# Kernel optimization log

Measured on AMD Instinct MI355X. Metric: run time of the kernel, lower is better.

Reference implementation:

```python
import jax, jax.numpy as jnp
import numpy as np

B, S, D = 16, 2048, 512
SEQ_START = 4
MAX_LEN = 1007
NUM_SEQ = MAX_LEN - SEQ_START  # 1003 rows in sequence_embeddings
VOCAB = 100


def setup_inputs() -> dict:
    key = jax.random.key(0)
    k_x, k_ids, k_pos, k_c, k_s = jax.random.split(key, 5)
    x = jax.random.normal(k_x, (B, S, D), dtype=jnp.float32)
    input_ids = jax.random.randint(k_ids, (B, S), 0, VOCAB, dtype=jnp.int64)
    start_token_id = 5
    # plant exactly one guaranteed start token per row at pos >= SEQ_START
    start_pos = jax.random.randint(k_pos, (B,), SEQ_START, S // 2, dtype=jnp.int64)
    input_ids = input_ids.at[jnp.arange(B), start_pos].set(start_token_id)
    control_emb = jax.random.normal(k_c, (SEQ_START, D), dtype=jnp.float32) * 0.02
    sequence_emb = jax.random.normal(k_s, (NUM_SEQ, D), dtype=jnp.float32) * 0.02
    return {"x": x, "input_ids": input_ids, "start_token_id": start_token_id,
            "control_emb": control_emb, "sequence_emb": sequence_emb}


def reference(x, input_ids, start_token_id, control_emb, sequence_emb):
    Bx, Sx, Dx = x.shape
    pos = jnp.arange(Sx)
    # control embeddings fill positions [0, SEQ_START)
    n_ctrl = control_emb.shape[0]
    ctrl_mask = pos < n_ctrl                                 # [S]
    ctrl_part = control_emb[jnp.clip(pos, 0, n_ctrl - 1)]    # [S, D]
    ctrl_part = jnp.where(ctrl_mask[:, None], ctrl_part, 0.0)
    # sequence embeddings: for each position i, rel = i - (last start pos <= i
    # with start pos >= SEQ_START); later starts overwrite earlier ones,
    # matching the torch loop's overwrite semantics.
    is_start = (input_ids == start_token_id) & (pos[None, :] >= SEQ_START)  # [B, S]
    marker = jnp.where(is_start, pos[None, :], -1)
    last_start = jax.lax.cummax(marker, axis=1)              # [B, S]
    rel = pos[None, :] - last_start                          # [B, S]
    n_seq = sequence_emb.shape[0]
    valid = (last_start >= 0) & (rel < n_seq)                # [B, S]
    seq_part = sequence_emb[jnp.clip(rel, 0, n_seq - 1)]     # [B, S, D]
    pos_emb = jnp.where(valid[:, :, None], seq_part, ctrl_part[None, :, :])
    return x + pos_emb
```

## Files before the change

### kernel.cpp

```cpp
#include <hip/hip_runtime.h>
#include <hip/hip_bf16.h>


#define S_LEN 2048
#define D_DIM 512
#define D4 (D_DIM / 4)
#define SEQ_START 4
#define NUM_SEQ 1003
#define CS 64
#define NCHUNK (S_LEN / CS)
#define THREADS 512
#define NWAVE (THREADS / 64)
#define PER (S_LEN / THREADS)

typedef float f4 __attribute__((ext_vector_type(4)));

__global__ void __launch_bounds__(THREADS)
alpe_fused_kernel(const f4* __restrict__ x,
                  const f4* __restrict__ ctrl,
                  const f4* __restrict__ seq,
                  const int* __restrict__ ids,
                  const int* __restrict__ start_tok,
                  f4* __restrict__ out) {
    const int b   = blockIdx.x / NCHUNK;
    const int cid = blockIdx.x % NCHUNK;
    const int chunk_start = cid * CS;
    const int t = threadIdx.x;
    const int st = *start_tok;

    __shared__ int wmax[NWAVE];
    __shared__ int codes_s[CS];

    int m = -1;
    #pragma unroll
    for (int k = 0; k < PER; ++k) {
        const int j = t * PER + k;
        if (j < chunk_start) {
            const int id = ids[b * S_LEN + j];
            if (id == st && j >= SEQ_START) m = max(m, j);
        }
    }
    #pragma unroll
    for (int off = 32; off >= 1; off >>= 1)
        m = max(m, __shfl_xor(m, off));
    if ((t & 63) == 0) wmax[t >> 6] = m;
    __syncthreads();

    if (t < 64) {
        const int p = chunk_start + t;
        const int id = ids[b * S_LEN + p];
        int mk = (id == st && p >= SEQ_START) ? p : -1;
        #pragma unroll
        for (int off = 1; off < 64; off <<= 1) {
            const int o = __shfl_up(mk, off);
            if (t >= off) mk = max(mk, o);
        }
        int carry = -1;
        #pragma unroll
        for (int w = 0; w < NWAVE; ++w) carry = max(carry, wmax[w]);
        const int last = max(mk, carry);
        int code;
        if (last >= 0) {
            const int rel = p - last;
            code = (rel < NUM_SEQ) ? rel : -1;
        } else {
            code = (p < SEQ_START) ? (-2 - p) : -1;
        }
        codes_s[t] = code;
    }
    __syncthreads();

    const size_t base4 = ((size_t)(b * S_LEN + chunk_start)) * D4;
    #pragma unroll
    for (int it = 0; it < (CS * D4) / THREADS; ++it) {
        const int j  = it * THREADS + t;
        const int sl = j >> 7;
        const int d4 = j & (D4 - 1);
        const int code = codes_s[sl];
        const f4 xv = x[base4 + j];
        f4 e = (f4){0.f, 0.f, 0.f, 0.f};
        if (code >= 0) {
            e = seq[code * D4 + d4];
        } else if (code <= -2) {
            e = ctrl[(-2 - code) * D4 + d4];
        }
        out[base4 + j] = xv + e;
    }
}

extern "C" void kernel_launch(void* const* d_in, const int* in_sizes, int n_in,
                              void* d_out, int out_size, void* d_ws, size_t ws_size,
                              hipStream_t stream) {
    const float* x         = (const float*)d_in[0];
    const int*   input_ids = (const int*)d_in[1];
    const int*   start_tok = (const int*)d_in[2];
    const float* ctrl      = (const float*)d_in[3];
    const float* seq       = (const float*)d_in[4];
    float*       out       = (float*)d_out;

    const int B = in_sizes[1] / S_LEN;
    const int grid = B * NCHUNK;

    alpe_fused_kernel<<<grid, THREADS, 0, stream>>>(
        (const f4*)x, (const f4*)ctrl, (const f4*)seq,
        input_ids, start_tok, (f4*)out);
}
```

Measured before the change: 27.15 us.

## Remove shared-memory syncs, compute codes per wave, and prefetch x rows early

```diff
diff --git a/kernel.cpp b/kernel.cpp
--- a/kernel.cpp
+++ b/kernel.cpp
@@ -3,88 +3,92 @@
 
 
 #define S_LEN 2048
-#define D_DIM 512
-#define D4 (D_DIM / 4)
+#define D4 128
 #define SEQ_START 4
 #define NUM_SEQ 1003
 #define CS 64
 #define NCHUNK (S_LEN / CS)
 #define THREADS 512
-#define NWAVE (THREADS / 64)
-#define PER (S_LEN / THREADS)
+#define ITERS ((CS * D4) / THREADS)
+#define PF 8
+#define IDR 8
 
 typedef float f4 __attribute__((ext_vector_type(4)));
+typedef int   i4 __attribute__((ext_vector_type(4)));
 
-__global__ void __launch_bounds__(THREADS)
-alpe_fused_kernel(const f4* __restrict__ x,
-                  const f4* __restrict__ ctrl,
-                  const f4* __restrict__ seq,
-                  const int* __restrict__ ids,
-                  const int* __restrict__ start_tok,
-                  f4* __restrict__ out) {
+__global__ void __launch_bounds__(THREADS, 4)
+alpe_kernel(const f4* __restrict__ x,
+            const f4* __restrict__ ctrl,
+            const f4* __restrict__ seq,
+            const int* __restrict__ ids,
+            const int* __restrict__ start_tok,
+            f4* __restrict__ out) {
     const int b   = blockIdx.x / NCHUNK;
     const int cid = blockIdx.x % NCHUNK;
     const int chunk_start = cid * CS;
     const int t = threadIdx.x;
+    const int w = t >> 6;
+    const int l = t & 63;
     const int st = *start_tok;
+    const int* __restrict__ idrow = ids + b * S_LEN;
 
-    __shared__ int wmax[NWAVE];
-    __shared__ int codes_s[CS];
+    const int myid = idrow[chunk_start + l];
+    i4 idv[IDR];
+    #pragma unroll
+    for (int r = 0; r < IDR; ++r)
+        idv[r] = *(const i4*)&idrow[r * 256 + l * 4];
 
-    int m = -1;
+    const size_t base4 = (size_t)(b * S_LEN + chunk_start) * D4;
+    f4 xp[PF];
     #pragma unroll
-    for (int k = 0; k < PER; ++k) {
-        const int j = t * PER + k;
-        if (j < chunk_start) {
-            const int id = ids[b * S_LEN + j];
-            if (id == st && j >= SEQ_START) m = max(m, j);
+    for (int i = 0; i < PF; ++i)
+        xp[i] = x[base4 + i * THREADS + t];
+
+    int pm = -1;
+    #pragma unroll
+    for (int r = 0; r < IDR; ++r) {
+        #pragma unroll
+        for (int k = 0; k < 4; ++k) {
+            const int j = r * 256 + l * 4 + k;
+            const int id = idv[r][k];
+            if (id == st && j >= SEQ_START && j < chunk_start) pm = max(pm, j);
         }
     }
     #pragma unroll
     for (int off = 32; off >= 1; off >>= 1)
-        m = max(m, __shfl_xor(m, off));
-    if ((t & 63) == 0) wmax[t >> 6] = m;
-    __syncthreads();
+        pm = max(pm, __shfl_xor(pm, off));
 
-    if (t < 64) {
-        const int p = chunk_start + t;
-        const int id = ids[b * S_LEN + p];
-        int mk = (id == st && p >= SEQ_START) ? p : -1;
-        #pragma unroll
-        for (int off = 1; off < 64; off <<= 1) {
-            const int o = __shfl_up(mk, off);
-            if (t >= off) mk = max(mk, o);
-        }
-        int carry = -1;
-        #pragma unroll
-        for (int w = 0; w < NWAVE; ++w) carry = max(carry, wmax[w]);
-        const int last = max(mk, carry);
-        int code;
-        if (last >= 0) {
-            const int rel = p - last;
-            code = (rel < NUM_SEQ) ? rel : -1;
-        } else {
-            code = (p < SEQ_START) ? (-2 - p) : -1;
-        }
-        codes_s[t] = code;
+    const int p = chunk_start + l;
+    int mk = (myid == st && p >= SEQ_START) ? p : -1;
+    #pragma unroll
+    for (int off = 1; off < 64; off <<= 1) {
+        const int o = __shfl_up(mk, off);
+        if (l >= off) mk = max(mk, o);
     }
-    __syncthreads();
+    const int last = max(mk, pm);
+    int mycode;
+    if (last >= 0) {
+        const int rel = p - last;
+        mycode = (rel < NUM_SEQ) ? rel : -1;
+    } else {
+        mycode = (p < SEQ_START) ? (-2 - p) : -1;
+    }
 
-    const size_t base4 = ((size_t)(b * S_LEN + chunk_start)) * D4;
+    const int d4w = ((w & 1) << 6) | l;
+    const int rsel = w >> 1;
     #pragma unroll
-    for (int it = 0; it < (CS * D4) / THREADS; ++it) {
-        const int j  = it * THREADS + t;
-        const int sl = j >> 7;
-        const int d4 = j & (D4 - 1);
-        const int code = codes_s[sl];
-        const f4 xv = x[base4 + j];
+    for (int it = 0; it < ITERS; ++it) {
+        const f4 xv = xp[it & (PF - 1)];
+        if (it + PF < ITERS)
+            xp[it & (PF - 1)] = x[base4 + (it + PF) * THREADS + t];
+        const int code = __shfl(mycode, 4 * it + rsel);
         f4 e = (f4){0.f, 0.f, 0.f, 0.f};
         if (code >= 0) {
-            e = seq[code * D4 + d4];
+            e = seq[code * D4 + d4w];
         } else if (code <= -2) {
-            e = ctrl[(-2 - code) * D4 + d4];
+            e = ctrl[(-2 - code) * D4 + d4w];
         }
-        out[base4 + j] = xv + e;
+        out[base4 + it * THREADS + t] = xv + e;
     }
 }
 
@@ -101,7 +105,7 @@
     const int B = in_sizes[1] / S_LEN;
     const int grid = B * NCHUNK;
 
-    alpe_fused_kernel<<<grid, THREADS, 0, stream>>>(
+    alpe_kernel<<<grid, THREADS, 0, stream>>>(
         (const f4*)x, (const f4*)ctrl, (const f4*)seq,
         input_ids, start_tok, (f4*)out);
 }
```

Measured after the change: 25.65 us, median of 2. -5.5%, faster.
